# Kernel optimization log

Hardware: AMD Instinct MI355X
Metric: run time of the kernel (lower is better)

The kernel has to match this reference:

```python
import jax, jax.numpy as jnp
import numpy as np

NUM_NEG = 100            # number of negative samples per masked step
CLAMP_W = 1.0            # clamped_logit_weight
B, C, T, M = 8, 256, 1024, 512


def setup_inputs() -> dict:
    key = jax.random.key(0)
    k1, k2, k3 = jax.random.split(key, 3)
    feat_proj = jax.random.normal(k1, (B, C, T), dtype=jnp.float32)
    context_output = jax.random.normal(k2, (B, C, T), dtype=jnp.float32)
    # exactly M masked timesteps per batch row (random positions)
    perm = jax.vmap(lambda k: jax.random.permutation(k, T))(jax.random.split(k3, B))
    mask = perm < M  # [B, T] bool, M True per row
    return {"feat_proj": feat_proj, "mask": mask,
            "context_output": context_output, "num_masked": M}


def reference(feat_proj, mask, context_output, num_masked):
    Bb, Cc, Tt = feat_proj.shape
    # indices of masked timesteps, in time order (stable argsort) -> [B, M]
    idx = jnp.argsort(jnp.logical_not(mask), axis=1)[:, :num_masked]
    feat_t = jnp.swapaxes(feat_proj, 1, 2)        # [B, T, C]
    ctx_t = jnp.swapaxes(context_output, 1, 2)    # [B, T, C]
    mf = jnp.take_along_axis(feat_t, idx[:, :, None], axis=1)  # [B, M, C]
    mc = jnp.take_along_axis(ctx_t, idx[:, :, None], axis=1)   # [B, M, C]
    # uniform sampling of NUM_NEG negatives without replacement, excluding self:
    # random scores per (t, candidate), self set to -1, take top-k
    scores = jax.random.uniform(jax.random.key(42), (Bb, num_masked, num_masked))
    self_mask = jnp.eye(num_masked, dtype=bool)
    scores = jnp.where(self_mask[None], -1.0, scores)
    _, neg_idx = jax.lax.top_k(scores, NUM_NEG)                 # [B, M, K]
    neg_feats = jnp.take_along_axis(mf[:, None, :, :], neg_idx[..., None], axis=2)  # [B, M, K, C]
    pos_logit = jnp.einsum('bmc,bmc->bm', mc, mf)               # [B, M]
    neg_logit = jnp.einsum('bmc,bmkc->bmk', mc, neg_feats)      # [B, M, K]
    logits = jnp.concatenate([pos_logit[..., None], neg_logit], axis=-1)  # [B, M, 1+K]
    total_loss = jnp.sum(jax.nn.softmax(logits, axis=-1)[..., 0])
    clamped = CLAMP_W * jnp.tanh(logits / CLAMP_W)
    total_aux_loss = jnp.sum(clamped ** 2)
    return total_loss, total_aux_loss
```

## Files before the change

kernel.cpp:

```cpp
#include <hip/hip_runtime.h>
#include <stdint.h>

#define NB   8
#define NC   256
#define NT   1024
#define NM   512
#define NNEG 100

typedef unsigned short u16;
typedef unsigned long long u64;
typedef __attribute__((ext_vector_type(8))) short bf16x8;
typedef __attribute__((ext_vector_type(4))) float f32x4;

#define WAVE_LDS_FENCE() asm volatile("s_waitcnt lgkmcnt(0)" ::: "memory")

__device__ __forceinline__ unsigned rotl32(unsigned x, int d) {
  return (x << d) | (x >> (32 - d));
}

__device__ unsigned threefry_bits(unsigned i) {
  const unsigned half = 1048576u;
  const bool lo = i < half;
  unsigned v0 = lo ? i : (i - half);
  unsigned v1 = lo ? (i + half) : i;
  const unsigned k0 = 0u, k1 = 42u;
  const unsigned k2 = k0 ^ k1 ^ 0x1BD11BDAu;
  v0 += k0; v1 += k1;
#define TF_R(r) { v0 += v1; v1 = rotl32(v1, r); v1 ^= v0; }
  TF_R(13) TF_R(15) TF_R(26) TF_R(6)
  v0 += k1; v1 += k2 + 1u;
  TF_R(17) TF_R(29) TF_R(16) TF_R(24)
  v0 += k2; v1 += k0 + 2u;
  TF_R(13) TF_R(15) TF_R(26) TF_R(6)
  v0 += k0; v1 += k1 + 3u;
  TF_R(17) TF_R(29) TF_R(16) TF_R(24)
  v0 += k1; v1 += k2 + 4u;
  TF_R(13) TF_R(15) TF_R(26) TF_R(6)
  v0 += k2; v1 += k0 + 5u;
#undef TF_R
  return lo ? v0 : v1;
}

__global__ __launch_bounds__(256) void k_compact(const float* __restrict__ ctx,
                                                 const float* __restrict__ feat,
                                                 const void* __restrict__ maskp,
                                                 u16* __restrict__ MC, u16* __restrict__ MF,
                                                 int* __restrict__ counter) {
  __shared__ float lds[64][129];
  __shared__ int posl[128];
  __shared__ int wsum[4];
  __shared__ int det[3];
  const int tid = threadIdx.x;
  const int lane = tid & 63, wid = tid >> 6;
  const int t0 = blockIdx.x * 128;
  const int b = blockIdx.y >> 1, mat = blockIdx.y & 1;
  const unsigned char* mb = (const unsigned char*)maskp;

  if (blockIdx.x == 0 && blockIdx.y == 0 && tid == 0) *counter = 0;

  if (tid < 3) det[tid] = 0;
  __syncthreads();
  {
    int c1 = 0, c4 = 0, c8 = 0;
    for (int j = tid; j < 1024; j += 256) {
      c1 += (mb[j] != 0);
      c4 += (((const unsigned*)mb)[j] != 0u);
      c8 += (((const u64*)mb)[j] != 0ull);
    }
#pragma unroll
    for (int off = 32; off; off >>= 1) {
      c1 += __shfl_xor(c1, off, 64);
      c4 += __shfl_xor(c4, off, 64);
      c8 += __shfl_xor(c8, off, 64);
    }
    if (lane == 0) { atomicAdd(&det[0], c1); atomicAdd(&det[1], c4); atomicAdd(&det[2], c8); }
  }
  __syncthreads();
  const int stride = (det[1] == 512) ? 4 : ((det[0] == 512) ? 1 : ((det[2] == 512) ? 8 : 4));

  int f4[4]; int s = 0;
#pragma unroll
  for (int j = 0; j < 4; ++j) {
    int tt = 4 * tid + j;
    size_t e = (size_t)b * NT + tt;
    int f;
    if (stride == 1)      f = (mb[e] != 0);
    else if (stride == 4) f = (((const unsigned*)mb)[e] != 0u);
    else                  f = (((const u64*)mb)[e] != 0ull);
    f4[j] = f; s += f;
  }
  int incl = s;
#pragma unroll
  for (int off = 1; off < 64; off <<= 1) {
    int o = __shfl_up(incl, off, 64);
    if (lane >= off) incl += o;
  }
  if (lane == 63) wsum[wid] = incl;
  __syncthreads();
  int wbase = 0;
#pragma unroll
  for (int w = 0; w < 4; ++w) if (w < wid) wbase += wsum[w];
  int excl = wbase + incl - s;
#pragma unroll
  for (int j = 0; j < 4; ++j) {
    int tt = 4 * tid + j;
    if (tt >= t0 && tt < t0 + 128) posl[tt - t0] = f4[j] ? excl : -1;
    excl += f4[j];
  }

  const float* src = (mat ? feat : ctx) + (size_t)b * NC * NT;
  u16* dst = (mat ? MF : MC) + (size_t)b * NM * NC;

  const int c4i = tid >> 6, tl = tid & 63, tr = tid >> 6;
  for (int chunk = 0; chunk < 4; ++chunk) {
    int c0 = chunk * 64;
    __syncthreads();
    for (int ci = 0; ci < 16; ++ci) {
      int cc = c4i * 16 + ci;
#pragma unroll
      for (int tj = 0; tj < 2; ++tj) {
        int tt = tl + 64 * tj;
        lds[cc][tt] = src[(size_t)(c0 + cc) * NT + t0 + tt];
      }
    }
    __syncthreads();
    for (int tt = tr; tt < 128; tt += 4) {
      int p = posl[tt];
      if (p >= 0) {
        unsigned xb = __float_as_uint(lds[tl][tt]);
        xb += 0x7FFFu + ((xb >> 16) & 1u);
        dst[(size_t)p * NC + c0 + tl] = (u16)(xb >> 16);
      }
    }
  }
}

__global__ __launch_bounds__(256) void k_fused(const u16* __restrict__ MC,
                                               const u16* __restrict__ MF,
                                               float* __restrict__ partials,
                                               int* __restrict__ counter,
                                               float* __restrict__ out) {
  __shared__ float S_lds[16][516];
  __shared__ unsigned hist[4][256];
  __shared__ u64 bk[4][32];
  __shared__ int bcnt[4], bbin[4], bneed[4];
  __shared__ unsigned char sf[4][512];
  __shared__ float wred[4][2];
  __shared__ int slast;

  const int tid = threadIdx.x;
  const int lane = tid & 63, wv = tid >> 6;
  const int bid = blockIdx.x;
  const int b = bid >> 5, m0 = (bid & 31) * 16;
  const int r16 = lane & 15, g = lane >> 4;

  {
    const u16* Arow = MC + ((size_t)(b * NM + m0 + r16)) * NC + g * 8;
    bf16x8 a[8];
#pragma unroll
    for (int ks = 0; ks < 8; ++ks) a[ks] = *(const bf16x8*)(Arow + ks * 32);

    const u16* Bbase = MF + ((size_t)(b * NM + wv * 128 + r16)) * NC + g * 8;
    f32x4 zero = {0.f, 0.f, 0.f, 0.f};
    f32x4 acc[8];
#pragma unroll
    for (int n = 0; n < 8; ++n) acc[n] = zero;

#pragma unroll
    for (int ks = 0; ks < 8; ++ks) {
#pragma unroll
      for (int n = 0; n < 8; ++n) {
        bf16x8 bv = *(const bf16x8*)(Bbase + (size_t)n * 16 * NC + ks * 32);
        acc[n] = __builtin_amdgcn_mfma_f32_16x16x32_bf16(a[ks], bv, acc[n], 0, 0, 0);
      }
    }

#pragma unroll
    for (int n = 0; n < 8; ++n)
#pragma unroll
      for (int q = 0; q < 4; ++q)
        S_lds[g * 4 + q][wv * 128 + n * 16 + r16] = acc[n][q];
  }
  __syncthreads();

  float wsum_pl = 0.f, wsum_pa = 0.f;
  for (int rr = 0; rr < 4; ++rr) {
    const int rloc = wv * 4 + rr;
    const int m = m0 + rloc;
    const int row = b * NM + m;

#pragma unroll
    for (int q = 0; q < 4; ++q) hist[wv][lane * 4 + q] = 0;
#pragma unroll
    for (int j = 0; j < 8; ++j) sf[wv][j * 64 + lane] = 0;
    if (lane == 0) bcnt[wv] = 0;

    unsigned keys[8]; int bins[8]; bool selfj[8];
#pragma unroll
    for (int j = 0; j < 8; ++j) {
      int t = j * 64 + lane;
      unsigned bits = threefry_bits((unsigned)row * 512u + (unsigned)t);
      unsigned u = bits >> 9;
      keys[j] = (u << 9) | (unsigned)(511 - t);
      bins[j] = (int)(u >> 15);
      selfj[j] = (t == m);
      if (!selfj[j]) atomicAdd(&hist[wv][bins[j]], 1u);
    }
    WAVE_LDS_FENCE();

    {
      unsigned h0 = hist[wv][4 * lane + 0], h1 = hist[wv][4 * lane + 1];
      unsigned h2 = hist[wv][4 * lane + 2], h3 = hist[wv][4 * lane + 3];
      unsigned s = h0 + h1 + h2 + h3;
      unsigned suf = s;
#pragma unroll
      for (int off = 1; off < 64; off <<= 1) {
        unsigned o = __shfl_down(suf, off, 64);
        if (lane + off < 64) suf += o;
      }
      unsigned a3 = suf - s;
      unsigned a2 = a3 + h3;
      unsigned a1 = a2 + h2;
      unsigned a0 = a1 + h1;
      if (a3 < NNEG && a3 + h3 >= NNEG) { bbin[wv] = 4 * lane + 3; bneed[wv] = NNEG - (int)a3; }
      if (a2 < NNEG && a2 + h2 >= NNEG) { bbin[wv] = 4 * lane + 2; bneed[wv] = NNEG - (int)a2; }
      if (a1 < NNEG && a1 + h1 >= NNEG) { bbin[wv] = 4 * lane + 1; bneed[wv] = NNEG - (int)a1; }
      if (a0 < NNEG && a0 + h0 >= NNEG) { bbin[wv] = 4 * lane + 0; bneed[wv] = NNEG - (int)a0; }
    }
    WAVE_LDS_FENCE();

    const int bb = bbin[wv];
#pragma unroll
    for (int j = 0; j < 8; ++j) {
      if (!selfj[j] && bins[j] == bb) {
        int p = atomicAdd(&bcnt[wv], 1);
        bk[wv][p & 31] = (((u64)keys[j]) << 1) | 1ull;
      }
    }
    WAVE_LDS_FENCE();

    if (lane == 0) {
      int cnt = bcnt[wv]; if (cnt > 32) cnt = 32;
      int need = bneed[wv];
      for (int it = 0; it < need; ++it) {
        u64 best = 0ull; int bi = 0;
        for (int q = 0; q < cnt; ++q)
          if (bk[wv][q] > best) { best = bk[wv][q]; bi = q; }
        bk[wv][bi] = 0ull;
        int tt = 511 - (int)((best >> 1) & 511ull);
        sf[wv][tt] = 1;
      }
    }
    WAVE_LDS_FENCE();

    float lv[8]; bool act[8];
    float mv = -3.4e38f;
#pragma unroll
    for (int j = 0; j < 8; ++j) {
      lv[j] = S_lds[rloc][j * 64 + lane];
      act[j] = selfj[j] || (bins[j] > bb && !selfj[j]) || (sf[wv][j * 64 + lane] != 0);
      if (act[j]) mv = fmaxf(mv, lv[j]);
    }
#pragma unroll
    for (int off = 32; off > 0; off >>= 1) mv = fmaxf(mv, __shfl_xor(mv, off, 64));

    float es = 0.f, as = 0.f, ps = 0.f;
#pragma unroll
    for (int j = 0; j < 8; ++j) {
      if (act[j]) {
        float e = __expf(lv[j] - mv);
        float th = 1.f - 2.f / (__expf(2.f * lv[j]) + 1.f);
        es += e; as += th * th;
        if (selfj[j]) ps = e;
      }
    }
#pragma unroll
    for (int off = 32; off > 0; off >>= 1) {
      es += __shfl_xor(es, off, 64);
      as += __shfl_xor(as, off, 64);
      ps += __shfl_xor(ps, off, 64);
    }
    if (lane == 0) { wsum_pl += ps / es; wsum_pa += as; }
    WAVE_LDS_FENCE();
  }

  if (lane == 0) { wred[wv][0] = wsum_pl; wred[wv][1] = wsum_pa; }
  __syncthreads();

  if (tid == 0) {
    float bpl = wred[0][0] + wred[1][0] + wred[2][0] + wred[3][0];
    float bpa = wred[0][1] + wred[1][1] + wred[2][1] + wred[3][1];
    partials[2 * bid] = bpl;
    partials[2 * bid + 1] = bpa;
    __threadfence();
    int old = atomicAdd(counter, 1);
    slast = (old == 255);
  }
  __syncthreads();
  if (slast) {
    __threadfence();
    float* s1 = (float*)hist;
    float* s2 = s1 + 256;
    s1[tid] = partials[2 * tid];
    s2[tid] = partials[2 * tid + 1];
    __syncthreads();
    for (int off = 128; off > 0; off >>= 1) {
      if (tid < off) { s1[tid] += s1[tid + off]; s2[tid] += s2[tid + off]; }
      __syncthreads();
    }
    if (tid == 0) { out[0] = s1[0]; out[1] = s2[0]; }
  }
}

extern "C" void kernel_launch(void* const* d_in, const int* in_sizes, int n_in,
                              void* d_out, int out_size, void* d_ws, size_t ws_size,
                              hipStream_t stream) {
  const float* feat = (const float*)d_in[0];
  const void*  mask = d_in[1];
  const float* ctx  = (const float*)d_in[2];
  float* out = (float*)d_out;

  char* ws = (char*)d_ws;
  u16*   MC      = (u16*)ws;
  u16*   MF      = (u16*)(ws + (2u << 20));
  float* partials = (float*)(ws + (4u << 20));
  int*   counter  = (int*)(ws + (4u << 20) + 4096);

  dim3 gc(NT / 128, NB * 2);
  k_compact<<<gc, 256, 0, stream>>>(ctx, feat, mask, MC, MF, counter);

  k_fused<<<NB * 32, 256, 0, stream>>>(MC, MF, partials, counter, out);
}
```

Baseline: 59.34 us.

## Split fused kernel into LDS-tiled GEMM and per-row loss kernel

The fused GEMM-plus-loss kernel is split into two kernels. The first is a 64x64-tiled bf16 MFMA GEMM with double-buffered LDS staging that writes the full score matrix S to global memory. The second is a loss kernel that gives each wave one row, so 512 blocks run in parallel instead of 256 blocks each looping over four rows. This is meant to raise parallelism and reuse of MF tiles, at the cost of an extra launch and an 8 MB fp32 write and read of S through global memory.

```diff
diff --git a/kernel.cpp b/kernel.cpp
--- a/kernel.cpp
+++ b/kernel.cpp
@@ -135,176 +135,205 @@
   }
 }
 
-__global__ __launch_bounds__(256) void k_fused(const u16* __restrict__ MC,
-                                               const u16* __restrict__ MF,
-                                               float* __restrict__ partials,
-                                               int* __restrict__ counter,
-                                               float* __restrict__ out) {
-  __shared__ float S_lds[16][516];
-  __shared__ unsigned hist[4][256];
-  __shared__ u64 bk[4][32];
-  __shared__ int bcnt[4], bbin[4], bneed[4];
-  __shared__ unsigned char sf[4][512];
-  __shared__ float wred[4][2];
+__global__ __launch_bounds__(256) void k_gemm(const u16* __restrict__ MC,
+                                              const u16* __restrict__ MF,
+                                              float* __restrict__ S) {
+  __shared__ u16 smem[2][5120];
+  const int tid = threadIdx.x;
+  const int b = blockIdx.z, m0 = blockIdx.y * 64, j0 = blockIdx.x * 64;
+  const int wave = tid >> 6, lane = tid & 63;
+  const int wm = wave >> 1, wn = wave & 1;
+  const int r = lane & 15, g = lane >> 4;
+
+  const int srow = tid >> 2, sq = tid & 3;
+  const u16* Asrc = MC + (size_t)(b * NM + m0 + srow) * NC + sq * 8;
+  const u16* Bsrc = MF + (size_t)(b * NM + j0 + srow) * NC + sq * 8;
+  const int sdst = srow * 40 + sq * 8;
+
+  uint4 ra, rb;
+  auto load_regs = [&](int c0) {
+    ra = *(const uint4*)(Asrc + c0);
+    rb = *(const uint4*)(Bsrc + c0);
+  };
+  auto write_lds = [&](int buf) {
+    *(uint4*)(smem[buf] + sdst) = ra;
+    *(uint4*)(smem[buf] + 2560 + sdst) = rb;
+  };
+
+  f32x4 zero = {0.f, 0.f, 0.f, 0.f};
+  f32x4 acc[2][2];
+#pragma unroll
+  for (int m = 0; m < 2; ++m)
+#pragma unroll
+    for (int n = 0; n < 2; ++n) acc[m][n] = zero;
+
+  load_regs(0);
+  write_lds(0);
+  __syncthreads();
+
+  for (int ks = 0; ks < 8; ++ks) {
+    const int cur = ks & 1;
+    if (ks < 7) load_regs((ks + 1) * 32);
+    const u16* base = smem[cur];
+    bf16x8 a[2], bvv[2];
+#pragma unroll
+    for (int m = 0; m < 2; ++m)
+      a[m] = *(const bf16x8*)(base + (wm * 32 + m * 16 + r) * 40 + g * 8);
+#pragma unroll
+    for (int n = 0; n < 2; ++n)
+      bvv[n] = *(const bf16x8*)(base + 2560 + (wn * 32 + n * 16 + r) * 40 + g * 8);
+#pragma unroll
+    for (int m = 0; m < 2; ++m)
+#pragma unroll
+      for (int n = 0; n < 2; ++n)
+        acc[m][n] = __builtin_amdgcn_mfma_f32_16x16x32_bf16(a[m], bvv[n], acc[m][n], 0, 0, 0);
+    if (ks < 7) write_lds(cur ^ 1);
+    __syncthreads();
+  }
+
+  float* Sb = S + (size_t)b * NM * NM;
+#pragma unroll
+  for (int m = 0; m < 2; ++m)
+#pragma unroll
+    for (int n = 0; n < 2; ++n)
+#pragma unroll
+      for (int q = 0; q < 4; ++q) {
+        int rowi = m0 + wm * 32 + m * 16 + g * 4 + q;
+        int col  = j0 + wn * 32 + n * 16 + r;
+        Sb[(size_t)rowi * NM + col] = acc[m][n][q];
+      }
+}
+
+__global__ __launch_bounds__(512) void k_loss(const float* __restrict__ S,
+                                              float* __restrict__ partials,
+                                              int* __restrict__ counter,
+                                              float* __restrict__ out) {
+  __shared__ unsigned hist[8][256];
+  __shared__ u64 bk[8][32];
+  __shared__ int bcnt[8], bbin[8], bneed[8];
+  __shared__ unsigned char sf[8][512];
+  __shared__ float wred[8][2];
   __shared__ int slast;
 
   const int tid = threadIdx.x;
   const int lane = tid & 63, wv = tid >> 6;
-  const int bid = blockIdx.x;
-  const int b = bid >> 5, m0 = (bid & 31) * 16;
-  const int r16 = lane & 15, g = lane >> 4;
+  const int row = blockIdx.x * 8 + wv;
+  const int m = row & (NM - 1);
+
+#pragma unroll
+  for (int q = 0; q < 4; ++q) hist[wv][lane * 4 + q] = 0;
+#pragma unroll
+  for (int j = 0; j < 8; ++j) sf[wv][j * 64 + lane] = 0;
+  if (lane == 0) bcnt[wv] = 0;
+
+  unsigned keys[8]; int bins[8]; bool selfj[8];
+#pragma unroll
+  for (int j = 0; j < 8; ++j) {
+    int t = j * 64 + lane;
+    unsigned bits = threefry_bits((unsigned)row * 512u + (unsigned)t);
+    unsigned u = bits >> 9;
+    keys[j] = (u << 9) | (unsigned)(511 - t);
+    bins[j] = (int)(u >> 15);
+    selfj[j] = (t == m);
+    if (!selfj[j]) atomicAdd(&hist[wv][bins[j]], 1u);
+  }
+  WAVE_LDS_FENCE();
 
   {
-    const u16* Arow = MC + ((size_t)(b * NM + m0 + r16)) * NC + g * 8;
-    bf16x8 a[8];
-#pragma unroll
-    for (int ks = 0; ks < 8; ++ks) a[ks] = *(const bf16x8*)(Arow + ks * 32);
-
-    const u16* Bbase = MF + ((size_t)(b * NM + wv * 128 + r16)) * NC + g * 8;
-    f32x4 zero = {0.f, 0.f, 0.f, 0.f};
-    f32x4 acc[8];
-#pragma unroll
-    for (int n = 0; n < 8; ++n) acc[n] = zero;
-
-#pragma unroll
-    for (int ks = 0; ks < 8; ++ks) {
-#pragma unroll
-      for (int n = 0; n < 8; ++n) {
-        bf16x8 bv = *(const bf16x8*)(Bbase + (size_t)n * 16 * NC + ks * 32);
-        acc[n] = __builtin_amdgcn_mfma_f32_16x16x32_bf16(a[ks], bv, acc[n], 0, 0, 0);
-      }
-    }
-
-#pragma unroll
-    for (int n = 0; n < 8; ++n)
-#pragma unroll
-      for (int q = 0; q < 4; ++q)
-        S_lds[g * 4 + q][wv * 128 + n * 16 + r16] = acc[n][q];
-  }
-  __syncthreads();
-
-  float wsum_pl = 0.f, wsum_pa = 0.f;
-  for (int rr = 0; rr < 4; ++rr) {
-    const int rloc = wv * 4 + rr;
-    const int m = m0 + rloc;
-    const int row = b * NM + m;
-
-#pragma unroll
-    for (int q = 0; q < 4; ++q) hist[wv][lane * 4 + q] = 0;
-#pragma unroll
-    for (int j = 0; j < 8; ++j) sf[wv][j * 64 + lane] = 0;
-    if (lane == 0) bcnt[wv] = 0;
-
-    unsigned keys[8]; int bins[8]; bool selfj[8];
-#pragma unroll
-    for (int j = 0; j < 8; ++j) {
-      int t = j * 64 + lane;
-      unsigned bits = threefry_bits((unsigned)row * 512u + (unsigned)t);
-      unsigned u = bits >> 9;
-      keys[j] = (u << 9) | (unsigned)(511 - t);
-      bins[j] = (int)(u >> 15);
-      selfj[j] = (t == m);
-      if (!selfj[j]) atomicAdd(&hist[wv][bins[j]], 1u);
-    }
-    WAVE_LDS_FENCE();
-
-    {
-      unsigned h0 = hist[wv][4 * lane + 0], h1 = hist[wv][4 * lane + 1];
-      unsigned h2 = hist[wv][4 * lane + 2], h3 = hist[wv][4 * lane + 3];
-      unsigned s = h0 + h1 + h2 + h3;
-      unsigned suf = s;
-#pragma unroll
-      for (int off = 1; off < 64; off <<= 1) {
-        unsigned o = __shfl_down(suf, off, 64);
-        if (lane + off < 64) suf += o;
-      }
-      unsigned a3 = suf - s;
-      unsigned a2 = a3 + h3;
-      unsigned a1 = a2 + h2;
-      unsigned a0 = a1 + h1;
-      if (a3 < NNEG && a3 + h3 >= NNEG) { bbin[wv] = 4 * lane + 3; bneed[wv] = NNEG - (int)a3; }
-      if (a2 < NNEG && a2 + h2 >= NNEG) { bbin[wv] = 4 * lane + 2; bneed[wv] = NNEG - (int)a2; }
-      if (a1 < NNEG && a1 + h1 >= NNEG) { bbin[wv] = 4 * lane + 1; bneed[wv] = NNEG - (int)a1; }
-      if (a0 < NNEG && a0 + h0 >= NNEG) { bbin[wv] = 4 * lane + 0; bneed[wv] = NNEG - (int)a0; }
-    }
-    WAVE_LDS_FENCE();
-
-    const int bb = bbin[wv];
-#pragma unroll
-    for (int j = 0; j < 8; ++j) {
-      if (!selfj[j] && bins[j] == bb) {
-        int p = atomicAdd(&bcnt[wv], 1);
-        bk[wv][p & 31] = (((u64)keys[j]) << 1) | 1ull;
-      }
-    }
-    WAVE_LDS_FENCE();
-
-    if (lane == 0) {
-      int cnt = bcnt[wv]; if (cnt > 32) cnt = 32;
-      int need = bneed[wv];
-      for (int it = 0; it < need; ++it) {
-        u64 best = 0ull; int bi = 0;
-        for (int q = 0; q < cnt; ++q)
-          if (bk[wv][q] > best) { best = bk[wv][q]; bi = q; }
-        bk[wv][bi] = 0ull;
-        int tt = 511 - (int)((best >> 1) & 511ull);
-        sf[wv][tt] = 1;
-      }
-    }
-    WAVE_LDS_FENCE();
-
-    float lv[8]; bool act[8];
-    float mv = -3.4e38f;
-#pragma unroll
-    for (int j = 0; j < 8; ++j) {
-      lv[j] = S_lds[rloc][j * 64 + lane];
-      act[j] = selfj[j] || (bins[j] > bb && !selfj[j]) || (sf[wv][j * 64 + lane] != 0);
-      if (act[j]) mv = fmaxf(mv, lv[j]);
-    }
-#pragma unroll
-    for (int off = 32; off > 0; off >>= 1) mv = fmaxf(mv, __shfl_xor(mv, off, 64));
-
-    float es = 0.f, as = 0.f, ps = 0.f;
-#pragma unroll
-    for (int j = 0; j < 8; ++j) {
-      if (act[j]) {
-        float e = __expf(lv[j] - mv);
-        float th = 1.f - 2.f / (__expf(2.f * lv[j]) + 1.f);
-        es += e; as += th * th;
-        if (selfj[j]) ps = e;
-      }
-    }
-#pragma unroll
-    for (int off = 32; off > 0; off >>= 1) {
-      es += __shfl_xor(es, off, 64);
-      as += __shfl_xor(as, off, 64);
-      ps += __shfl_xor(ps, off, 64);
-    }
-    if (lane == 0) { wsum_pl += ps / es; wsum_pa += as; }
-    WAVE_LDS_FENCE();
-  }
-
-  if (lane == 0) { wred[wv][0] = wsum_pl; wred[wv][1] = wsum_pa; }
+    unsigned h0 = hist[wv][4 * lane + 0], h1 = hist[wv][4 * lane + 1];
+    unsigned h2 = hist[wv][4 * lane + 2], h3 = hist[wv][4 * lane + 3];
+    unsigned s = h0 + h1 + h2 + h3;
+    unsigned suf = s;
+#pragma unroll
+    for (int off = 1; off < 64; off <<= 1) {
+      unsigned o = __shfl_down(suf, off, 64);
+      if (lane + off < 64) suf += o;
+    }
+    unsigned a3 = suf - s;
+    unsigned a2 = a3 + h3;
+    unsigned a1 = a2 + h2;
+    unsigned a0 = a1 + h1;
+    if (a3 < NNEG && a3 + h3 >= NNEG) { bbin[wv] = 4 * lane + 3; bneed[wv] = NNEG - (int)a3; }
+    if (a2 < NNEG && a2 + h2 >= NNEG) { bbin[wv] = 4 * lane + 2; bneed[wv] = NNEG - (int)a2; }
+    if (a1 < NNEG && a1 + h1 >= NNEG) { bbin[wv] = 4 * lane + 1; bneed[wv] = NNEG - (int)a1; }
+    if (a0 < NNEG && a0 + h0 >= NNEG) { bbin[wv] = 4 * lane + 0; bneed[wv] = NNEG - (int)a0; }
+  }
+  WAVE_LDS_FENCE();
+
+  const int bb = bbin[wv];
+#pragma unroll
+  for (int j = 0; j < 8; ++j) {
+    if (!selfj[j] && bins[j] == bb) {
+      int p = atomicAdd(&bcnt[wv], 1);
+      bk[wv][p & 31] = (((u64)keys[j]) << 1) | 1ull;
+    }
+  }
+  WAVE_LDS_FENCE();
+
+  if (lane == 0) {
+    int cnt = bcnt[wv]; if (cnt > 32) cnt = 32;
+    int need = bneed[wv];
+    for (int it = 0; it < need; ++it) {
+      u64 best = 0ull; int bi = 0;
+      for (int q = 0; q < cnt; ++q)
+        if (bk[wv][q] > best) { best = bk[wv][q]; bi = q; }
+      bk[wv][bi] = 0ull;
+      int tt = 511 - (int)((best >> 1) & 511ull);
+      sf[wv][tt] = 1;
+    }
+  }
+  WAVE_LDS_FENCE();
+
+  const float* Srow = S + (size_t)row * NM;
+  float lv[8]; bool act[8];
+  float mv = -3.4e38f;
+#pragma unroll
+  for (int j = 0; j < 8; ++j) {
+    lv[j] = Srow[j * 64 + lane];
+    act[j] = selfj[j] || (bins[j] > bb && !selfj[j]) || (sf[wv][j * 64 + lane] != 0);
+    if (act[j]) mv = fmaxf(mv, lv[j]);
+  }
+#pragma unroll
+  for (int off = 32; off > 0; off >>= 1) mv = fmaxf(mv, __shfl_xor(mv, off, 64));
+
+  float es = 0.f, as = 0.f, ps = 0.f;
+#pragma unroll
+  for (int j = 0; j < 8; ++j) {
+    if (act[j]) {
+      float e = __expf(lv[j] - mv);
+      float th = 1.f - 2.f / (__expf(2.f * lv[j]) + 1.f);
+      es += e; as += th * th;
+      if (selfj[j]) ps = e;
+    }
+  }
+#pragma unroll
+  for (int off = 32; off > 0; off >>= 1) {
+    es += __shfl_xor(es, off, 64);
+    as += __shfl_xor(as, off, 64);
+    ps += __shfl_xor(ps, off, 64);
+  }
+  if (lane == 0) { wred[wv][0] = ps / es; wred[wv][1] = as; }
   __syncthreads();
 
   if (tid == 0) {
-    float bpl = wred[0][0] + wred[1][0] + wred[2][0] + wred[3][0];
-    float bpa = wred[0][1] + wred[1][1] + wred[2][1] + wred[3][1];
-    partials[2 * bid] = bpl;
-    partials[2 * bid + 1] = bpa;
+    float bpl = 0.f, bpa = 0.f;
+#pragma unroll
+    for (int w = 0; w < 8; ++w) { bpl += wred[w][0]; bpa += wred[w][1]; }
+    partials[2 * blockIdx.x] = bpl;
+    partials[2 * blockIdx.x + 1] = bpa;
     __threadfence();
     int old = atomicAdd(counter, 1);
-    slast = (old == 255);
+    slast = (old == 511);
   }
   __syncthreads();
   if (slast) {
     __threadfence();
     float* s1 = (float*)hist;
-    float* s2 = s1 + 256;
+    float* s2 = s1 + 512;
     s1[tid] = partials[2 * tid];
     s2[tid] = partials[2 * tid + 1];
     __syncthreads();
-    for (int off = 128; off > 0; off >>= 1) {
+    for (int off = 256; off > 0; off >>= 1) {
       if (tid < off) { s1[tid] += s1[tid + off]; s2[tid] += s2[tid + off]; }
       __syncthreads();
     }
@@ -321,13 +350,17 @@
   float* out = (float*)d_out;
 
   char* ws = (char*)d_ws;
-  u16*   MC      = (u16*)ws;
-  u16*   MF      = (u16*)(ws + (2u << 20));
-  float* partials = (float*)(ws + (4u << 20));
-  int*   counter  = (int*)(ws + (4u << 20) + 4096);
+  u16*   MC       = (u16*)ws;
+  u16*   MF       = (u16*)(ws + (2u << 20));
+  float* S        = (float*)(ws + (4u << 20));
+  float* partials = (float*)(ws + (12u << 20));
+  int*   counter  = (int*)(ws + (12u << 20) + 8192);
 
   dim3 gc(NT / 128, NB * 2);
   k_compact<<<gc, 256, 0, stream>>>(ctx, feat, mask, MC, MF, counter);
 
-  k_fused<<<NB * 32, 256, 0, stream>>>(MC, MF, partials, counter, out);
-}
+  dim3 g2(NM / 64, NM / 64, NB);
+  k_gemm<<<g2, 256, 0, stream>>>(MC, MF, S);
+
+  k_loss<<<NB * NM / 8, 512, 0, stream>>>(S, partials, counter, out);
+}
```

Result: faster. 54.92 us (-7.4%).
